# Kernel tuning notes

Measured on AMD Instinct MI355X. Metric: run time of the kernel, lower is better.

Reference implementation:

```python
import jax, jax.numpy as jnp
import numpy as np

B, H, S, D = 4, 32, 4096, 128      # max_batch_size, n_heads, max_seq_length, head_dim
HC = 1024                          # heavy_const (gathered tokens per head)
S_NEW = 512                        # tokens written per update call


def setup_inputs() -> dict:
    key = jax.random.key(0)
    k0, k1, k2, k3, k4 = jax.random.split(key, 5)
    # Pinned-CPU caches (buffers) materialized as plain arrays
    k_cache = jax.random.normal(k0, (B, H, S, D), dtype=jnp.float32)
    v_cache = jax.random.normal(k1, (B, H, S, D), dtype=jnp.float32)
    # New KV chunk being written
    k_val = jax.random.normal(k2, (B, H, S_NEW, D), dtype=jnp.float32)
    v_val = jax.random.normal(k3, (B, H, S_NEW, D), dtype=jnp.float32)
    # Positions being updated (distinct, so scatter is well-defined)
    input_pos = jnp.arange(S_NEW, dtype=jnp.int32)
    # Flattened row indices into the (B*H*S, D) view of the cache
    flatten_index = jax.random.randint(k4, (B * H * HC,), 0, B * H * S, dtype=jnp.int32)
    return {
        "k_cache": k_cache, "v_cache": v_cache,
        "k_val": k_val, "v_val": v_val,
        "input_pos": input_pos, "flatten_index": flatten_index,
    }


def reference(k_cache, v_cache, k_val, v_val, input_pos, flatten_index):
    # update(): indexed scatter of the new chunk into the full caches
    k_cache = k_cache.at[:, :, input_pos].set(k_val)
    v_cache = v_cache.at[:, :, input_pos].set(v_val)
    # load_gpu(): gather heavy-hitter rows from the flattened (-1, D) view
    d = k_cache.shape[-1]
    k_gpu = k_cache.reshape(-1, d)[flatten_index].reshape(B, H, HC, d)
    v_gpu = v_cache.reshape(-1, d)[flatten_index].reshape(B, H, HC, d)
    # stack K/V gathered caches -> [2, B, H, HC, D]
    return jnp.stack([k_gpu, v_gpu])
```

## Files before the change

kernel.cpp:

```cpp
#include <hip/hip_runtime.h>

constexpr int B     = 4;
constexpr int H     = 32;
constexpr int S     = 4096;
constexpr int D     = 128;
constexpr int HC    = 1024;
constexpr int S_NEW = 512;

constexpr int NROWS = B * H * HC;
constexpr int VPR   = D / 4;
constexpr int LOG_VPR   = 5;
constexpr int LOG_S     = 12;
constexpr unsigned TOTAL = (unsigned)NROWS * VPR;

typedef float f32x4 __attribute__((ext_vector_type(4)));

__global__ void build_inverse_map(const int* __restrict__ input_pos,
                                  int* __restrict__ pos2slot) {
    for (int i = threadIdx.x; i < S; i += blockDim.x) pos2slot[i] = -1;
    __syncthreads();
    if (threadIdx.x < S_NEW) pos2slot[input_pos[threadIdx.x]] = (int)threadIdx.x;
}

__global__ __launch_bounds__(256) void gather_kernel(
    const f32x4* __restrict__ k_cache, const f32x4* __restrict__ v_cache,
    const f32x4* __restrict__ k_val,   const f32x4* __restrict__ v_val,
    const int* __restrict__ fidx, const int* __restrict__ pos2slot,
    f32x4* __restrict__ out)
{
    unsigned tid = blockIdx.x * blockDim.x + threadIdx.x;
    unsigned vec = tid & (VPR - 1);
    unsigned row = tid >> LOG_VPR;

    int r  = fidx[row];
    int s  = r & (S - 1);
    int bh = r >> LOG_S;

    int slot = pos2slot[s];

    const f32x4* ksrc;
    const f32x4* vsrc;
    if (slot >= 0) {
        size_t off = ((size_t)bh * S_NEW + (size_t)slot) * VPR + vec;
        ksrc = k_val + off;
        vsrc = v_val + off;
    } else {
        size_t off = (size_t)r * VPR + vec;
        ksrc = k_cache + off;
        vsrc = v_cache + off;
    }
    f32x4 kq = *ksrc;
    f32x4 vq = *vsrc;
    __builtin_nontemporal_store(kq, out + tid);
    __builtin_nontemporal_store(vq, out + TOTAL + tid);
}

extern "C" void kernel_launch(void* const* d_in, const int* in_sizes, int n_in,
                              void* d_out, int out_size, void* d_ws, size_t ws_size,
                              hipStream_t stream) {
    const float* k_cache   = (const float*)d_in[0];
    const float* v_cache   = (const float*)d_in[1];
    const float* k_val     = (const float*)d_in[2];
    const float* v_val     = (const float*)d_in[3];
    const int*   input_pos = (const int*)d_in[4];
    const int*   fidx      = (const int*)d_in[5];
    f32x4*       out       = (f32x4*)d_out;

    int* pos2slot = (int*)d_ws;

    build_inverse_map<<<1, 512, 0, stream>>>(input_pos, pos2slot);

    unsigned blocks = TOTAL / 256u;
    gather_kernel<<<blocks, 256, 0, stream>>>(
        (const f32x4*)k_cache, (const f32x4*)v_cache,
        (const f32x4*)k_val,   (const f32x4*)v_val,
        fidx, pos2slot, out);
}
```

Baseline: 49.59 us.

## Fuse inverse-map build into gather kernel and process two rows per thread

Removes the separate single-block kernel that builds the position-to-slot map. Each gather block now rebuilds the 4096-entry map in shared memory. Each thread also handles two rows, which halves the grid and doubles the loads in flight per thread. The cost is that every block redundantly initialises 16KB of LDS and syncs twice before it can start gathering.

```diff
diff --git a/kernel.cpp b/kernel.cpp
--- a/kernel.cpp
+++ b/kernel.cpp
@@ -9,50 +9,57 @@
 
 constexpr int NROWS = B * H * HC;
 constexpr int VPR   = D / 4;
-constexpr int LOG_VPR   = 5;
-constexpr int LOG_S     = 12;
+constexpr int LOG_VPR = 5;
+constexpr int LOG_S   = 12;
 constexpr unsigned TOTAL = (unsigned)NROWS * VPR;
+constexpr unsigned HALF  = TOTAL / 2;
+constexpr int BLOCK = 256;
 
 typedef float f32x4 __attribute__((ext_vector_type(4)));
 
-__global__ void build_inverse_map(const int* __restrict__ input_pos,
-                                  int* __restrict__ pos2slot) {
-    for (int i = threadIdx.x; i < S; i += blockDim.x) pos2slot[i] = -1;
-    __syncthreads();
-    if (threadIdx.x < S_NEW) pos2slot[input_pos[threadIdx.x]] = (int)threadIdx.x;
-}
-
-__global__ __launch_bounds__(256) void gather_kernel(
+__global__ __launch_bounds__(BLOCK) void fused_gather(
     const f32x4* __restrict__ k_cache, const f32x4* __restrict__ v_cache,
     const f32x4* __restrict__ k_val,   const f32x4* __restrict__ v_val,
-    const int* __restrict__ fidx, const int* __restrict__ pos2slot,
+    const int* __restrict__ input_pos, const int* __restrict__ fidx,
     f32x4* __restrict__ out)
 {
-    unsigned tid = blockIdx.x * blockDim.x + threadIdx.x;
-    unsigned vec = tid & (VPR - 1);
-    unsigned row = tid >> LOG_VPR;
+    __shared__ int p2s[S];
+    #pragma unroll
+    for (int i = threadIdx.x; i < S; i += BLOCK) p2s[i] = -1;
+    __syncthreads();
+    #pragma unroll
+    for (int i = threadIdx.x; i < S_NEW; i += BLOCK) p2s[input_pos[i]] = i;
+    __syncthreads();
 
-    int r  = fidx[row];
-    int s  = r & (S - 1);
-    int bh = r >> LOG_S;
+    unsigned tid  = blockIdx.x * BLOCK + threadIdx.x;
+    unsigned vec  = tid & (VPR - 1);
+    unsigned row0 = tid >> LOG_VPR;
+    unsigned row1 = row0 + (NROWS >> 1);
 
-    int slot = pos2slot[s];
+    int r0 = fidx[row0];
+    int r1 = fidx[row1];
+    int s0 = r0 & (S - 1),  s1 = r1 & (S - 1);
+    int bh0 = r0 >> LOG_S,  bh1 = r1 >> LOG_S;
+    int sl0 = p2s[s0],      sl1 = p2s[s1];
 
-    const f32x4* ksrc;
-    const f32x4* vsrc;
-    if (slot >= 0) {
-        size_t off = ((size_t)bh * S_NEW + (size_t)slot) * VPR + vec;
-        ksrc = k_val + off;
-        vsrc = v_val + off;
-    } else {
-        size_t off = (size_t)r * VPR + vec;
-        ksrc = k_cache + off;
-        vsrc = v_cache + off;
-    }
-    f32x4 kq = *ksrc;
-    f32x4 vq = *vsrc;
-    __builtin_nontemporal_store(kq, out + tid);
-    __builtin_nontemporal_store(vq, out + TOTAL + tid);
+    size_t o0 = (sl0 >= 0) ? ((size_t)bh0 * S_NEW + (size_t)sl0) * VPR + vec
+                           : (size_t)r0 * VPR + vec;
+    size_t o1 = (sl1 >= 0) ? ((size_t)bh1 * S_NEW + (size_t)sl1) * VPR + vec
+                           : (size_t)r1 * VPR + vec;
+    const f32x4* kb0 = (sl0 >= 0) ? k_val : k_cache;
+    const f32x4* vb0 = (sl0 >= 0) ? v_val : v_cache;
+    const f32x4* kb1 = (sl1 >= 0) ? k_val : k_cache;
+    const f32x4* vb1 = (sl1 >= 0) ? v_val : v_cache;
+
+    f32x4 kq0 = kb0[o0];
+    f32x4 kq1 = kb1[o1];
+    f32x4 vq0 = vb0[o0];
+    f32x4 vq1 = vb1[o1];
+
+    __builtin_nontemporal_store(kq0, out + tid);
+    __builtin_nontemporal_store(kq1, out + HALF + tid);
+    __builtin_nontemporal_store(vq0, out + TOTAL + tid);
+    __builtin_nontemporal_store(vq1, out + TOTAL + HALF + tid);
 }
 
 extern "C" void kernel_launch(void* const* d_in, const int* in_sizes, int n_in,
@@ -66,13 +73,9 @@
     const int*   fidx      = (const int*)d_in[5];
     f32x4*       out       = (f32x4*)d_out;
 
-    int* pos2slot = (int*)d_ws;
-
-    build_inverse_map<<<1, 512, 0, stream>>>(input_pos, pos2slot);
-
-    unsigned blocks = TOTAL / 256u;
-    gather_kernel<<<blocks, 256, 0, stream>>>(
+    unsigned blocks = HALF / BLOCK;
+    fused_gather<<<blocks, BLOCK, 0, stream>>>(
         (const f32x4*)k_cache, (const f32x4*)v_cache,
         (const f32x4*)k_val,   (const f32x4*)v_val,
-        fidx, pos2slot, out);
+        input_pos, fidx, out);
 }
```

New measurement: 45.55 us. 8.2% less time.
